# Optimization experiments

Measured on AMD Instinct MI355X. Metric: run time of the kernel, lower is better.

Reference implementation:

```python
import jax, jax.numpy as jnp
import numpy as np

N, C, IN_DIM, H_DIM, NUM_DEP = 16384, 4, 300, 512, 48


def setup_inputs() -> dict:
    key = jax.random.key(0)
    ks = jax.random.split(key, 12)
    # --- tree structure: 4-ary heap, reversed so children have SMALLER index than parent; root = N-1 ---
    i = np.arange(N)
    j = (N - 1) - i                                   # heap index (root j=0)
    cj = C * j[:, None] + 1 + np.arange(C)[None, :]   # heap indices of children [N,C]
    valid = cj <= N - 1
    child_idx = np.where(valid, (N - 1) - cj, 0).astype(np.int32)
    mask_h = valid.astype(np.float32)
    mask_e = valid.astype(np.float32)
    rng = np.random.default_rng(0)
    child_dep = rng.integers(0, NUM_DEP, size=(N, C)).astype(np.int32)
    leaf = ~valid.any(axis=1)
    # torch leaf branch: one virtual child with h=zeros and dep index 0
    mask_e[leaf, 0] = 1.0
    child_dep[leaf, 0] = 0
    child_idx[leaf, 0] = 0
    s = 0.02  # weight scale (stands in for xavier init)
    lin = lambda k, o, d: (jax.random.normal(k, (o, d), jnp.float32) * s)
    return {
        "x": jax.random.normal(ks[0], (N, IN_DIM), jnp.float32),
        "child_idx": jnp.asarray(child_idx),
        "child_dep": jnp.asarray(child_dep),
        "mask_h": jnp.asarray(mask_h),
        "mask_e": jnp.asarray(mask_e),
        "demb": jax.random.normal(ks[1], (NUM_DEP, H_DIM), jnp.float32) * s,
        "iux_w": lin(ks[2], 2 * H_DIM, IN_DIM), "iux_b": jnp.zeros((2 * H_DIM,), jnp.float32),
        "iuh_w": lin(ks[3], 2 * H_DIM, H_DIM), "iuh_b": jnp.zeros((2 * H_DIM,), jnp.float32),
        "iue_w": lin(ks[4], 2 * H_DIM, H_DIM), "iue_b": jnp.zeros((2 * H_DIM,), jnp.float32),
        "fx_w": lin(ks[5], H_DIM, IN_DIM), "fx_b": jnp.zeros((H_DIM,), jnp.float32),
        "fh_w": lin(ks[6], H_DIM, H_DIM), "fh_b": jnp.zeros((H_DIM,), jnp.float32),
        "fe_w": lin(ks[7], H_DIM, H_DIM), "fe_b": jnp.zeros((H_DIM,), jnp.float32),
    }


def reference(x, child_idx, child_dep, mask_h, mask_e, demb,
              iux_w, iux_b, iuh_w, iuh_b, iue_w, iue_b,
              fx_w, fx_b, fh_w, fh_b, fe_w, fe_b):
    n, h_dim = x.shape[0], fh_w.shape[0]

    def step(H, xs):
        t, xt, cidx, cdep, mh, me = xs
        ch = H[cidx] * mh[:, None]            # [C,h] child hiddens (zeros for pad / leaf virtual child)
        e = demb[cdep]                        # [C,h] dependency embeddings
        h_sum = ch.sum(0)                     # child-sum h
        e_sum = (e * me[:, None]).sum(0)      # child-sum dep embedding (leaf -> demb[0])
        iu = (xt @ iux_w.T + iux_b) + (h_sum @ iuh_w.T + iuh_b) + (e_sum @ iue_w.T + iue_b)
        i_g = jax.nn.sigmoid(iu[:h_dim])
        u = jnp.tanh(iu[h_dim:])
        f = jax.nn.sigmoid(ch @ fh_w.T + fh_b + (xt @ fx_w.T + fx_b) + e @ fe_w.T + fe_b)  # [C,h]
        h_new = jnp.tanh(i_g * u + (f * ch).sum(0))   # padded rows contribute 0 since ch=0
        return H.at[t].set(h_new), None

    H0 = jnp.zeros((n, h_dim), x.dtype)
    xs = (jnp.arange(n), x, child_idx, child_dep, mask_h, mask_e)
    Hf, _ = jax.lax.scan(step, H0, xs)
    return Hf[n - 1][None, :]   # root hidden state, shape [1, h_dim]
```

## Files before the change

kernel.cpp:

```cpp
#include <hip/hip_runtime.h>
#include <cstddef>

#define N_NODES 16384
#define HD      512
#define INDIM   300
#define INP     320
#define NDEP    48
#define KT      32
#define LM      16
#define LCOL    128

typedef unsigned int u32;
typedef unsigned short u16;
typedef __attribute__((ext_vector_type(8))) short short8;
typedef __attribute__((ext_vector_type(4))) float f32x4;

typedef __attribute__((address_space(1))) const u32 as1_u32;
typedef __attribute__((address_space(3))) u32 as3_u32;

__device__ __forceinline__ float sigmoidf_(float v) {
    return 1.f / (1.f + __expf(-v));
}
__device__ __forceinline__ float tanhf_(float v) {
    v = fminf(15.f, fmaxf(-15.f, v));
    const float e = __expf(2.f * v);
    return (e - 1.f) / (e + 1.f);
}
__device__ __forceinline__ u16 f2bf(float f) {
    u32 u = __float_as_uint(f);
    u32 r = (u + 0x7fffu + ((u >> 16) & 1u)) >> 16;
    return (u16)r;
}

__global__ __launch_bounds__(256)
void emb_proj_kernel(const float* __restrict__ demb,
                     const float* __restrict__ iue_w,
                     const float* __restrict__ fe_w,
                     const float* __restrict__ iux_b,
                     const float* __restrict__ iuh_b,
                     const float* __restrict__ iue_b,
                     const float* __restrict__ fx_b,
                     const float* __restrict__ fh_b,
                     const float* __restrict__ fe_b,
                     float* __restrict__ iemb,
                     float* __restrict__ femb,
                     float* __restrict__ ibc,
                     float* __restrict__ fbc)
{
    const int bo  = blockIdx.x;
    const int tid = threadIdx.x;
    if (bo == 384) {
        for (int o = tid; o < 1024; o += 256) ibc[o] = iux_b[o] + iuh_b[o] + iue_b[o];
        for (int o = tid; o < 512;  o += 256) fbc[o] = fx_b[o] + fh_b[o] + fe_b[o];
        return;
    }
    const int wave = tid >> 6;
    const int d    = tid & 63;
    const bool isI = (bo < 256);
    const int o    = (isI ? bo : bo - 256) * 4 + wave;
    const float* wrow = isI ? (iue_w + (size_t)o * HD) : (fe_w + (size_t)o * HD);
    if (d >= NDEP) return;
    const float* drow = demb + (size_t)d * HD;

    float4 a0 = make_float4(0.f, 0.f, 0.f, 0.f);
    float4 a1 = make_float4(0.f, 0.f, 0.f, 0.f);
    for (int k = 0; k < HD; k += 8) {
        const float4 wv0 = *reinterpret_cast<const float4*>(wrow + k);
        const float4 wv1 = *reinterpret_cast<const float4*>(wrow + k + 4);
        const float4 dv0 = *reinterpret_cast<const float4*>(drow + k);
        const float4 dv1 = *reinterpret_cast<const float4*>(drow + k + 4);
        a0.x = fmaf(dv0.x, wv0.x, a0.x); a0.y = fmaf(dv0.y, wv0.y, a0.y);
        a0.z = fmaf(dv0.z, wv0.z, a0.z); a0.w = fmaf(dv0.w, wv0.w, a0.w);
        a1.x = fmaf(dv1.x, wv1.x, a1.x); a1.y = fmaf(dv1.y, wv1.y, a1.y);
        a1.z = fmaf(dv1.z, wv1.z, a1.z); a1.w = fmaf(dv1.w, wv1.w, a1.w);
    }
    const float s = ((a0.x + a0.y) + (a0.z + a0.w)) + ((a1.x + a1.y) + (a1.z + a1.w));
    if (isI) iemb[(size_t)d * 1024 + o] = s;
    else     femb[(size_t)d * 512  + o] = s;
}

__global__ __launch_bounds__(256)
void convert_pack_kernel(const float* __restrict__ w1, const float* __restrict__ w2,
                         u16* __restrict__ out, int n1, int K, int Kp, int total)
{
    const int idx = blockIdx.x * 256 + threadIdx.x;
    if (idx >= total) return;
    const int r = idx / Kp, k = idx - r * Kp;
    float v = 0.f;
    if (k < K) v = (r < n1) ? w1[(size_t)r * K + k] : w2[(size_t)(r - n1) * K + k];
    out[idx] = f2bf(v);
}

__device__ __forceinline__
void gemm_body(u16* As, u16* Bs,
               const u16* __restrict__ A, int lda,
               const u16* __restrict__ B, int ldb,
               float* __restrict__ C, int ldc,
               int M, int K, int bx, int by)
{
    const int tid  = threadIdx.x;
    const int lane = tid & 63;
    const int wave = tid >> 6;
    const int mBlk = bx * 128;
    const int nBlk = by * 128;

    const int wr = (wave >> 1) * 64;
    const int wc = (wave & 1) * 64;
    const int fr = lane & 15;
    const int kg = lane >> 4;

    f32x4 acc[4][4];
    #pragma unroll
    for (int i = 0; i < 4; ++i)
        #pragma unroll
        for (int j = 0; j < 4; ++j) acc[i][j] = (f32x4){0.f, 0.f, 0.f, 0.f};

    int offA[4], offB[4];
    #pragma unroll
    for (int it = 0; it < 4; ++it) {
        const int s   = it * 256 + tid;
        const int row = s >> 3, c = s & 7;
        const int cs  = c ^ (row & 7);
        int ga = mBlk + row; if (ga > M - 1) ga = M - 1;
        offA[it] = ga * lda + cs * 8;
        offB[it] = (nBlk + row) * ldb + cs * 8;
    }

    for (int k0 = 0; k0 < K; k0 += 64) {
        #pragma unroll
        for (int it = 0; it < 4; ++it) {
            const int ldsOff = (it * 256 + wave * 64) * 8;
            __builtin_amdgcn_global_load_lds((as1_u32*)(A + offA[it] + k0),
                                             (as3_u32*)(&As[ldsOff]), 16, 0, 0);
            __builtin_amdgcn_global_load_lds((as1_u32*)(B + offB[it] + k0),
                                             (as3_u32*)(&Bs[ldsOff]), 16, 0, 0);
        }
        __syncthreads();
        #pragma unroll
        for (int half = 0; half < 2; ++half) {
            const int ckb = half * 4 + kg;
            short8 af[4], bf[4];
            #pragma unroll
            for (int f = 0; f < 4; ++f) {
                const int ar = wr + f * 16 + fr;
                af[f] = *(const short8*)&As[ar * 64 + ((ckb ^ (ar & 7)) * 8)];
                const int br = wc + f * 16 + fr;
                bf[f] = *(const short8*)&Bs[br * 64 + ((ckb ^ (br & 7)) * 8)];
            }
            #pragma unroll
            for (int mi = 0; mi < 4; ++mi)
                #pragma unroll
                for (int ni = 0; ni < 4; ++ni)
                    acc[mi][ni] = __builtin_amdgcn_mfma_f32_16x16x32_bf16(
                                      af[mi], bf[ni], acc[mi][ni], 0, 0, 0);
        }
        __syncthreads();
    }

    #pragma unroll
    for (int mi = 0; mi < 4; ++mi) {
        const int r0 = mBlk + wr + mi * 16 + kg * 4;
        #pragma unroll
        for (int v = 0; v < 4; ++v) {
            const int r = r0 + v;
            if (r >= M) continue;
            float* crow = C + (size_t)r * ldc + nBlk + wc + fr;
            #pragma unroll
            for (int ni = 0; ni < 4; ++ni)
                crow[ni * 16] = acc[mi][ni][v];
        }
    }
}

__global__ __launch_bounds__(256, 2)
void gemm_bf16_kernel(const u16* __restrict__ A, int lda,
                      const u16* __restrict__ B, int ldb,
                      float* __restrict__ C, int ldc,
                      int M, int K)
{
    __shared__ u16 As[128 * 64];
    __shared__ u16 Bs[128 * 64];
    gemm_body(As, Bs, A, lda, B, ldb, C, ldc, M, K, blockIdx.x, blockIdx.y);
}

__global__ __launch_bounds__(256, 2)
void gemm_bf16_dual_kernel(const u16* __restrict__ A1, int lda1,
                           const u16* __restrict__ B1, int ldb1,
                           float* __restrict__ C1, int ldc1, int M1, int K1,
                           int gx1, int n1,
                           const u16* __restrict__ A2, int lda2,
                           const u16* __restrict__ B2, int ldb2,
                           float* __restrict__ C2, int ldc2, int M2, int K2,
                           int gx2)
{
    __shared__ u16 As[128 * 64];
    __shared__ u16 Bs[128 * 64];
    const int flat = blockIdx.x;
    if (flat < n1) {
        gemm_body(As, Bs, A1, lda1, B1, ldb1, C1, ldc1, M1, K1,
                  flat % gx1, flat / gx1);
    } else {
        const int f2 = flat - n1;
        gemm_body(As, Bs, A2, lda2, B2, ldb2, C2, ldc2, M2, K2,
                  f2 % gx2, f2 / gx2);
    }
}

__global__ __launch_bounds__(256)
void leaf_kernel(const float* __restrict__ XP, const float* __restrict__ iemb,
                 const float* __restrict__ ibc, float* __restrict__ H,
                 u16* __restrict__ Hb)
{
    const int t = blockIdx.x;
    int j = threadIdx.x;
    #pragma unroll
    for (int rep = 0; rep < 2; ++rep, j += 256) {
        const float iu_i = XP[(size_t)t * 1536 + j]       + iemb[j]       + ibc[j];
        const float iu_u = XP[(size_t)t * 1536 + 512 + j] + iemb[512 + j] + ibc[512 + j];
        const float h = tanhf_(sigmoidf_(iu_i) * tanhf_(iu_u));
        H[(size_t)t * 512 + j]  = h;
        Hb[(size_t)t * 512 + j] = f2bf(h);
    }
}

__global__ __launch_bounds__(256)
void hsum_kernel(const float* __restrict__ H, const int* __restrict__ cidx,
                 const float* __restrict__ mh, u16* __restrict__ HSB, int lo)
{
    const int t = lo + blockIdx.x;
    int ci[4]; float m4[4];
    #pragma unroll
    for (int c = 0; c < 4; ++c) { ci[c] = cidx[t * 4 + c]; m4[c] = mh[t * 4 + c]; }
    int j = threadIdx.x;
    #pragma unroll
    for (int rep = 0; rep < 2; ++rep, j += 256) {
        float s = 0.f;
        #pragma unroll
        for (int c = 0; c < 4; ++c)
            if (m4[c] != 0.f) s += m4[c] * H[(size_t)ci[c] * 512 + j];
        HSB[(size_t)blockIdx.x * 512 + j] = f2bf(s);
    }
}

__global__ __launch_bounds__(256)
void combine_kernel(const float* __restrict__ XP, const float* __restrict__ PIU,
                    const float* __restrict__ GF,
                    const int* __restrict__ cidx, const int* __restrict__ cdep,
                    const float* __restrict__ mh, const float* __restrict__ me,
                    const float* __restrict__ iemb, const float* __restrict__ femb,
                    const float* __restrict__ ibc, const float* __restrict__ fbc,
                    float* __restrict__ H, u16* __restrict__ Hb, int lo)
{
    const int t = lo + blockIdx.x;
    int ci[4], dp[4]; float m4[4], e4[4];
    #pragma unroll
    for (int c = 0; c < 4; ++c) {
        ci[c] = cidx[t * 4 + c]; dp[c] = cdep[t * 4 + c];
        m4[c] = mh[t * 4 + c];   e4[c] = me[t * 4 + c];
    }
    int j = threadIdx.x;
    #pragma unroll
    for (int rep = 0; rep < 2; ++rep, j += 256) {
        float ei = 0.f, eu = 0.f;
        #pragma unroll
        for (int c = 0; c < 4; ++c)
            if (e4[c] != 0.f) {
                const float* ie = iemb + (size_t)dp[c] * 1024;
                ei += e4[c] * ie[j];
                eu += e4[c] * ie[512 + j];
            }
        const float iu_i = XP[(size_t)t * 1536 + j] + PIU[(size_t)blockIdx.x * 1024 + j]
                         + ibc[j] + ei;
        const float iu_u = XP[(size_t)t * 1536 + 512 + j] + PIU[(size_t)blockIdx.x * 1024 + 512 + j]
                         + ibc[512 + j] + eu;
        const float xf = XP[(size_t)t * 1536 + 1024 + j] + fbc[j];
        float fcs = 0.f;
        #pragma unroll
        for (int c = 0; c < 4; ++c)
            if (m4[c] != 0.f) {
                const float fv = GF[(size_t)ci[c] * 512 + j] + xf + femb[(size_t)dp[c] * 512 + j];
                fcs += sigmoidf_(fv) * (m4[c] * H[(size_t)ci[c] * 512 + j]);
            }
        const float h = tanhf_(sigmoidf_(iu_i) * tanhf_(iu_u) + fcs);
        H[(size_t)t * 512 + j]  = h;
        Hb[(size_t)t * 512 + j] = f2bf(h);
    }
}

__global__ void copy_out_kernel(const float* __restrict__ H, float* __restrict__ out) {
    const int j = blockIdx.x * 256 + threadIdx.x;
    if (j < HD) out[j] = H[(size_t)(N_NODES - 1) * HD + j];
}

__global__ __launch_bounds__(256)
void emb_setup_kernel(const float* __restrict__ demb,
                      const float* __restrict__ iue_w,
                      const float* __restrict__ fe_w,
                      const float* __restrict__ iux_b,
                      const float* __restrict__ iuh_b,
                      const float* __restrict__ iue_b,
                      const float* __restrict__ fx_b,
                      const float* __restrict__ fh_b,
                      const float* __restrict__ fe_b,
                      float* __restrict__ iemb,
                      float* __restrict__ femb,
                      float* __restrict__ ibc,
                      float* __restrict__ fbc)
{
    const int d   = blockIdx.x;
    const int tid = threadIdx.x;
    __shared__ float sd[HD];
    sd[tid]       = demb[d * HD + tid];
    sd[tid + 256] = demb[d * HD + 256 + tid];
    __syncthreads();

    #pragma unroll
    for (int r = 0; r < 4; ++r) {
        const int o = r * 256 + tid;
        const float* w = iue_w + (size_t)o * HD;
        float acc = 0.f;
        for (int k = 0; k < HD; k += 4) {
            const float4 wv = *reinterpret_cast<const float4*>(w + k);
            acc += sd[k] * wv.x + sd[k + 1] * wv.y + sd[k + 2] * wv.z + sd[k + 3] * wv.w;
        }
        iemb[(size_t)d * 1024 + o] = acc;
    }
    #pragma unroll
    for (int r = 0; r < 2; ++r) {
        const int o = r * 256 + tid;
        const float* w = fe_w + (size_t)o * HD;
        float acc = 0.f;
        for (int k = 0; k < HD; k += 4) {
            const float4 wv = *reinterpret_cast<const float4*>(w + k);
            acc += sd[k] * wv.x + sd[k + 1] * wv.y + sd[k + 2] * wv.z + sd[k + 3] * wv.w;
        }
        femb[(size_t)d * HD + o] = acc;
    }
    if (d == 0) {
        #pragma unroll
        for (int r = 0; r < 4; ++r) { const int o = r * 256 + tid; ibc[o] = iux_b[o] + iuh_b[o] + iue_b[o]; }
        #pragma unroll
        for (int r = 0; r < 2; ++r) { const int o = r * 256 + tid; fbc[o] = fx_b[o] + fh_b[o] + fe_b[o]; }
    }
}

__global__ __launch_bounds__(256, 2)
void level_kernel(const float* __restrict__ x,
                  const int*   __restrict__ child_idx,
                  const int*   __restrict__ child_dep,
                  const float* __restrict__ mask_h,
                  const float* __restrict__ mask_e,
                  const float* __restrict__ iux_w,
                  const float* __restrict__ iuh_w,
                  const float* __restrict__ fx_w,
                  const float* __restrict__ fh_w,
                  const float* __restrict__ iemb,
                  const float* __restrict__ femb,
                  const float* __restrict__ ibc,
                  const float* __restrict__ fbc,
                  float* __restrict__ H,
                  int tLo, int tEnd)
{
    __shared__ __align__(16) float sA[KT][68];
    __shared__ float sWI[KT][LCOL + 1];
    __shared__ float sWU[KT][LCOL + 1];
    __shared__ float sWF[KT][LCOL + 1];
    __shared__ int   sCidx[LM][4];
    __shared__ float sMh[LM][4];
    __shared__ int   sDep[LM][4];
    __shared__ float sMe[LM][4];

    const int tid  = threadIdx.x;
    const int base = tLo + blockIdx.x * LM;
    const int j0   = blockIdx.y * LCOL;

    if (tid < LM * 4) {
        const int m = tid >> 2, c = tid & 3;
        const int t = base + m;
        const bool v = (t < tEnd);
        sCidx[m][c] = v ? child_idx[t * 4 + c] : 0;
        sMh[m][c]   = v ? mask_h[t * 4 + c]    : 0.f;
        sDep[m][c]  = v ? child_dep[t * 4 + c] : 0;
        sMe[m][c]   = v ? mask_e[t * 4 + c]    : 0.f;
    }

    const int jj = tid & 63;
    const int mg = tid >> 6;

    float acc_i[4][2], acc_u[4][2], acc_fx[4][2], acc_f[4][2][4];
    #pragma unroll
    for (int mm = 0; mm < 4; ++mm)
        #pragma unroll
        for (int c2 = 0; c2 < 2; ++c2) {
            acc_i[mm][c2] = 0.f; acc_u[mm][c2] = 0.f; acc_fx[mm][c2] = 0.f;
            #pragma unroll
            for (int c = 0; c < 4; ++c) acc_f[mm][c2][c] = 0.f;
        }

    __syncthreads();

    for (int k0 = 0; k0 < HD; k0 += KT) {
        #pragma unroll
        for (int it = 0; it < 2; ++it) {
            const int chunk = tid + it * 256;
            const int mc = chunk >> 3;
            const int kk = (chunk & 7) * 4;
            const int m = mc >> 2, c = mc & 3;
            const float mh = sMh[m][c];
            float4 v = make_float4(0.f, 0.f, 0.f, 0.f);
            if (mh != 0.f)
                v = *reinterpret_cast<const float4*>(H + (size_t)sCidx[m][c] * HD + k0 + kk);
            sA[kk + 0][mc] = v.x; sA[kk + 1][mc] = v.y; sA[kk + 2][mc] = v.z; sA[kk + 3][mc] = v.w;
        }
        #pragma unroll
        for (int it = 0; it < 4; ++it) {
            const int chunk = tid + it * 256;
            const int row = chunk >> 3;
            const int kk = (chunk & 7) * 4;
            const float4 vI = *reinterpret_cast<const float4*>(iuh_w + (size_t)(j0 + row) * HD + k0 + kk);
            const float4 vU = *reinterpret_cast<const float4*>(iuh_w + (size_t)(j0 + row + 512) * HD + k0 + kk);
            const float4 vF = *reinterpret_cast<const float4*>(fh_w  + (size_t)(j0 + row) * HD + k0 + kk);
            sWI[kk + 0][row] = vI.x; sWI[kk + 1][row] = vI.y; sWI[kk + 2][row] = vI.z; sWI[kk + 3][row] = vI.w;
            sWU[kk + 0][row] = vU.x; sWU[kk + 1][row] = vU.y; sWU[kk + 2][row] = vU.z; sWU[kk + 3][row] = vU.w;
            sWF[kk + 0][row] = vF.x; sWF[kk + 1][row] = vF.y; sWF[kk + 2][row] = vF.z; sWF[kk + 3][row] = vF.w;
        }
        __syncthreads();
        #pragma unroll 4
        for (int k = 0; k < KT; ++k) {
            const float wi0 = sWI[k][jj], wi1 = sWI[k][jj + 64];
            const float wu0 = sWU[k][jj], wu1 = sWU[k][jj + 64];
            const float wf0 = sWF[k][jj], wf1 = sWF[k][jj + 64];
            #pragma unroll
            for (int mm = 0; mm < 4; ++mm) {
                const int m = mg + mm * 4;
                const float4 cv = *reinterpret_cast<const float4*>(&sA[k][m * 4]);
                const float hs = (cv.x + cv.y) + (cv.z + cv.w);
                acc_i[mm][0] = fmaf(hs, wi0, acc_i[mm][0]);
                acc_i[mm][1] = fmaf(hs, wi1, acc_i[mm][1]);
                acc_u[mm][0] = fmaf(hs, wu0, acc_u[mm][0]);
                acc_u[mm][1] = fmaf(hs, wu1, acc_u[mm][1]);
                acc_f[mm][0][0] = fmaf(cv.x, wf0, acc_f[mm][0][0]);
                acc_f[mm][1][0] = fmaf(cv.x, wf1, acc_f[mm][1][0]);
                acc_f[mm][0][1] = fmaf(cv.y, wf0, acc_f[mm][0][1]);
                acc_f[mm][1][1] = fmaf(cv.y, wf1, acc_f[mm][1][1]);
                acc_f[mm][0][2] = fmaf(cv.z, wf0, acc_f[mm][0][2]);
                acc_f[mm][1][2] = fmaf(cv.z, wf1, acc_f[mm][1][2]);
                acc_f[mm][0][3] = fmaf(cv.w, wf0, acc_f[mm][0][3]);
                acc_f[mm][1][3] = fmaf(cv.w, wf1, acc_f[mm][1][3]);
            }
        }
        __syncthreads();
    }

    for (int k0 = 0; k0 < INDIM; k0 += KT) {
        if (tid < 128) {
            const int m = tid >> 3;
            const int kk = (tid & 7) * 4;
            const int t = base + m;
            float4 v = make_float4(0.f, 0.f, 0.f, 0.f);
            if (t < tEnd && (k0 + kk + 3) < INDIM)
                v = *reinterpret_cast<const float4*>(x + (size_t)t * INDIM + k0 + kk);
            sA[kk + 0][m] = v.x; sA[kk + 1][m] = v.y; sA[kk + 2][m] = v.z; sA[kk + 3][m] = v.w;
        }
        #pragma unroll
        for (int it = 0; it < 4; ++it) {
            const int chunk = tid + it * 256;
            const int row = chunk >> 3;
            const int kk = (chunk & 7) * 4;
            float4 vI = make_float4(0.f, 0.f, 0.f, 0.f), vU = vI, vF = vI;
            if ((k0 + kk + 3) < INDIM) {
                vI = *reinterpret_cast<const float4*>(iux_w + (size_t)(j0 + row) * INDIM + k0 + kk);
                vU = *reinterpret_cast<const float4*>(iux_w + (size_t)(j0 + row + 512) * INDIM + k0 + kk);
                vF = *reinterpret_cast<const float4*>(fx_w  + (size_t)(j0 + row) * INDIM + k0 + kk);
            }
            sWI[kk + 0][row] = vI.x; sWI[kk + 1][row] = vI.y; sWI[kk + 2][row] = vI.z; sWI[kk + 3][row] = vI.w;
            sWU[kk + 0][row] = vU.x; sWU[kk + 1][row] = vU.y; sWU[kk + 2][row] = vU.z; sWU[kk + 3][row] = vU.w;
            sWF[kk + 0][row] = vF.x; sWF[kk + 1][row] = vF.y; sWF[kk + 2][row] = vF.z; sWF[kk + 3][row] = vF.w;
        }
        __syncthreads();
        #pragma unroll 4
        for (int k = 0; k < KT; ++k) {
            const float wi0 = sWI[k][jj], wi1 = sWI[k][jj + 64];
            const float wu0 = sWU[k][jj], wu1 = sWU[k][jj + 64];
            const float wf0 = sWF[k][jj], wf1 = sWF[k][jj + 64];
            #pragma unroll
            for (int mm = 0; mm < 4; ++mm) {
                const float xv = sA[k][mg + mm * 4];
                acc_i[mm][0]  = fmaf(xv, wi0, acc_i[mm][0]);
                acc_i[mm][1]  = fmaf(xv, wi1, acc_i[mm][1]);
                acc_u[mm][0]  = fmaf(xv, wu0, acc_u[mm][0]);
                acc_u[mm][1]  = fmaf(xv, wu1, acc_u[mm][1]);
                acc_fx[mm][0] = fmaf(xv, wf0, acc_fx[mm][0]);
                acc_fx[mm][1] = fmaf(xv, wf1, acc_fx[mm][1]);
            }
        }
        __syncthreads();
    }

    #pragma unroll
    for (int mm = 0; mm < 4; ++mm) {
        const int m = mg + mm * 4;
        const int t = base + m;
        if (t >= tEnd) continue;
        #pragma unroll
        for (int c2 = 0; c2 < 2; ++c2) {
            const int j = j0 + c2 * 64 + jj;
            float emb_i = 0.f, emb_u = 0.f;
            #pragma unroll
            for (int c = 0; c < 4; ++c) {
                const float mev = sMe[m][c];
                if (mev != 0.f) {
                    const float* ie = iemb + (size_t)sDep[m][c] * 1024;
                    emb_i = fmaf(mev, ie[j], emb_i);
                    emb_u = fmaf(mev, ie[j + 512], emb_u);
                }
            }
            const float iu_i = acc_i[mm][c2] + ibc[j] + emb_i;
            const float iu_u = acc_u[mm][c2] + ibc[j + 512] + emb_u;
            const float ig = sigmoidf_(iu_i);
            const float uu = tanhf_(iu_u);
            float fcs = 0.f;
            #pragma unroll
            for (int c = 0; c < 4; ++c) {
                const float mh = sMh[m][c];
                if (mh != 0.f) {
                    const float fv = acc_f[mm][c2][c] + acc_fx[mm][c2] + fbc[j]
                                   + femb[(size_t)sDep[m][c] * HD + j];
                    const float fg = sigmoidf_(fv);
                    const float chj = H[(size_t)sCidx[m][c] * HD + j] * mh;
                    fcs = fmaf(fg, chj, fcs);
                }
            }
            H[(size_t)t * HD + j] = tanhf_(fmaf(ig, uu, fcs));
        }
    }
}

static const int lvlLo[8] = {0, 10923, 15019, 16043, 16299, 16363, 16379, 16383};
static const int lvlN[8]  = {10923, 4096, 1024, 256, 64, 16, 4, 1};

extern "C" void kernel_launch(void* const* d_in, const int* in_sizes, int n_in,
                              void* d_out, int out_size, void* d_ws, size_t ws_size,
                              hipStream_t stream)
{
    const float* x     = (const float*)d_in[0];
    const int*   cidx  = (const int*)  d_in[1];
    const int*   cdep  = (const int*)  d_in[2];
    const float* mh    = (const float*)d_in[3];
    const float* me    = (const float*)d_in[4];
    const float* demb  = (const float*)d_in[5];
    const float* iux_w = (const float*)d_in[6];
    const float* iux_b = (const float*)d_in[7];
    const float* iuh_w = (const float*)d_in[8];
    const float* iuh_b = (const float*)d_in[9];
    const float* iue_w = (const float*)d_in[10];
    const float* iue_b = (const float*)d_in[11];
    const float* fx_w  = (const float*)d_in[12];
    const float* fx_b  = (const float*)d_in[13];
    const float* fh_w  = (const float*)d_in[14];
    const float* fh_b  = (const float*)d_in[15];
    const float* fe_w  = (const float*)d_in[16];
    const float* fe_b  = (const float*)d_in[17];

    const size_t szH   = 33554432;
    const size_t szHb  = 16777216;
    const size_t szXP  = 100663296;
    const size_t szGF  = 33554432;
    const size_t szPIU = 16777216;
    const size_t szHSB = 4194304;
    const size_t szXB  = 10485760;
    const size_t szWX  = 983040;
    const size_t szWH  = 1572864;
    const size_t szIE  = 196608, szFE = 98304, szIB = 4096, szFB = 2048;
    const size_t need = szH + szHb + szXP + szGF + szPIU + szHSB + szXB + szWX + szWH
                      + szIE + szFE + szIB + szFB;

    if (ws_size >= need) {
        char* w = (char*)d_ws;
        float* H    = (float*)w;  w += szH;
        u16*   Hb   = (u16*)w;    w += szHb;
        float* XP   = (float*)w;  w += szXP;
        float* GF   = (float*)w;  w += szGF;
        float* PIU  = (float*)w;  w += szPIU;
        u16*   HSB  = (u16*)w;    w += szHSB;
        u16*   xb   = (u16*)w;    w += szXB;
        u16*   WXb  = (u16*)w;    w += szWX;
        u16*   WHb  = (u16*)w;    w += szWH;
        float* iemb = (float*)w;  w += szIE;
        float* femb = (float*)w;  w += szFE;
        float* ibc  = (float*)w;  w += szIB;
        float* fbc  = (float*)w;  w += szFB;

        {
            const int tot = N_NODES * INP;
            hipLaunchKernelGGL(convert_pack_kernel, dim3((tot + 255) / 256), dim3(256), 0, stream,
                               x, x, xb, N_NODES, INDIM, INP, tot);
        }
        {
            const int tot = 1536 * INP;
            hipLaunchKernelGGL(convert_pack_kernel, dim3((tot + 255) / 256), dim3(256), 0, stream,
                               iux_w, fx_w, WXb, 1024, INDIM, INP, tot);
        }
        {
            const int tot = 1536 * HD;
            hipLaunchKernelGGL(convert_pack_kernel, dim3((tot + 255) / 256), dim3(256), 0, stream,
                               iuh_w, fh_w, WHb, 1024, HD, HD, tot);
        }
        hipLaunchKernelGGL(emb_proj_kernel, dim3(385), dim3(256), 0, stream,
                           demb, iue_w, fe_w, iux_b, iuh_b, iue_b, fx_b, fh_b, fe_b,
                           iemb, femb, ibc, fbc);

        hipLaunchKernelGGL(gemm_bf16_kernel, dim3(N_NODES / 128, 1536 / 128), dim3(256), 0, stream,
                           xb, INP, WXb, INP, XP, 1536, N_NODES, INP);

        hipLaunchKernelGGL(leaf_kernel, dim3(lvlN[0]), dim3(256), 0, stream, XP, iemb, ibc, H, Hb);

        for (int l = 1; l < 8; ++l) {
            const int pLo = lvlLo[l - 1], pN = lvlN[l - 1];
            const int lo  = lvlLo[l],     n  = lvlN[l];
            hipLaunchKernelGGL(hsum_kernel, dim3(n), dim3(256), 0, stream, H, cidx, mh, HSB, lo);
            const int gx1 = (pN + 127) / 128, n1 = gx1 * (512 / 128);
            const int gx2 = (n + 127) / 128,  n2 = gx2 * (1024 / 128);
            hipLaunchKernelGGL(gemm_bf16_dual_kernel, dim3(n1 + n2), dim3(256), 0, stream,
                               Hb + (size_t)pLo * HD, HD, WHb + (size_t)1024 * HD, HD,
                               GF + (size_t)pLo * HD, HD, pN, HD, gx1, n1,
                               HSB, HD, WHb, HD, PIU, 1024, n, HD, gx2);
            hipLaunchKernelGGL(combine_kernel, dim3(n), dim3(256), 0, stream,
                               XP, PIU, GF, cidx, cdep, mh, me, iemb, femb, ibc, fbc, H, Hb, lo);
        }
        hipLaunchKernelGGL(copy_out_kernel, dim3(2), dim3(256), 0, stream, H, (float*)d_out);
        return;
    }

    float* ws   = (float*)d_ws;
    float* H    = ws;
    float* iemb = H + (size_t)N_NODES * HD;
    float* femb = iemb + (size_t)NDEP * 1024;
    float* ibc  = femb + (size_t)NDEP * HD;
    float* fbc  = ibc + 1024;

    hipLaunchKernelGGL(emb_setup_kernel, dim3(NDEP), dim3(256), 0, stream,
                       demb, iue_w, fe_w, iux_b, iuh_b, iue_b, fx_b, fh_b, fe_b,
                       iemb, femb, ibc, fbc);
    for (int l = 0; l < 8; ++l) {
        dim3 grid((lvlN[l] + LM - 1) / LM, HD / LCOL);
        hipLaunchKernelGGL(level_kernel, grid, dim3(256), 0, stream,
                           x, cidx, cdep, mh, me, iux_w, iuh_w, fx_w, fh_w,
                           iemb, femb, ibc, fbc, H, lvlLo[l], lvlLo[l] + lvlN[l]);
    }
    hipLaunchKernelGGL(copy_out_kernel, dim3(2), dim3(256), 0, stream, H, (float*)d_out);
}
```

Baseline: 267.5 us.

## Fuse child-sum into combine, store GEMM outputs as bf16, merge conversion launches

Each level's combine is now launched per parent of the next level, computing its children's hidden states and writing the child-sum straight into the next GEMM's input. This removes the separate hsum kernel, the leaf kernel, the copy-out kernel and two of three conversion launches. GEMM outputs (XP, GF, PIU) are stored as bf16, and the forget-gate x projection is computed only for non-leaf rows, which cuts memory traffic. The cost is extra rounding in the intermediates, plus less parallelism in the upper levels, since one block now handles up to four children one after another.

```diff
diff --git a/kernel.cpp b/kernel.cpp
--- a/kernel.cpp
+++ b/kernel.cpp
@@ -6,6 +6,7 @@
 #define INDIM   300
 #define INP     320
 #define NDEP    48
+#define NLEAF   10923
 #define KT      32
 #define LM      16
 #define LCOL    128
@@ -30,6 +31,12 @@
     u32 u = __float_as_uint(f);
     u32 r = (u + 0x7fffu + ((u >> 16) & 1u)) >> 16;
     return (u16)r;
+}
+__device__ __forceinline__ float b2f(u16 v) {
+    return __uint_as_float((u32)v << 16);
+}
+__device__ __forceinline__ u32 pack2(float a, float b) {
+    return (u32)f2bf(a) | ((u32)f2bf(b) << 16);
 }
 
 __global__ __launch_bounds__(256)
@@ -79,23 +86,41 @@
     else     femb[(size_t)d * 512  + o] = s;
 }
 
+#define CV_T0 (N_NODES * INP)
+#define CV_T1 (1536 * INP)
+#define CV_T2 (1536 * HD)
+
 __global__ __launch_bounds__(256)
-void convert_pack_kernel(const float* __restrict__ w1, const float* __restrict__ w2,
-                         u16* __restrict__ out, int n1, int K, int Kp, int total)
+void convert_all_kernel(const float* __restrict__ x,
+                        const float* __restrict__ iux_w, const float* __restrict__ fx_w,
+                        const float* __restrict__ iuh_w, const float* __restrict__ fh_w,
+                        u16* __restrict__ xb, u16* __restrict__ WXb, u16* __restrict__ WHb)
 {
     const int idx = blockIdx.x * 256 + threadIdx.x;
-    if (idx >= total) return;
-    const int r = idx / Kp, k = idx - r * Kp;
-    float v = 0.f;
-    if (k < K) v = (r < n1) ? w1[(size_t)r * K + k] : w2[(size_t)(r - n1) * K + k];
-    out[idx] = f2bf(v);
+    if (idx < CV_T0) {
+        const int r = idx / INP, k = idx - r * INP;
+        xb[idx] = f2bf(k < INDIM ? x[(size_t)r * INDIM + k] : 0.f);
+    } else if (idx < CV_T0 + CV_T1) {
+        const int i2 = idx - CV_T0;
+        const int r = i2 / INP, k = i2 - r * INP;
+        float v = 0.f;
+        if (k < INDIM) v = (r < 1024) ? iux_w[(size_t)r * INDIM + k]
+                                      : fx_w[(size_t)(r - 1024) * INDIM + k];
+        WXb[i2] = f2bf(v);
+    } else {
+        const int i3 = idx - CV_T0 - CV_T1;
+        const int r = i3 >> 9, k = i3 & 511;
+        const float v = (r < 1024) ? iuh_w[(size_t)r * HD + k]
+                                   : fh_w[(size_t)(r - 1024) * HD + k];
+        WHb[i3] = f2bf(v);
+    }
 }
 
 __device__ __forceinline__
 void gemm_body(u16* As, u16* Bs,
                const u16* __restrict__ A, int lda,
                const u16* __restrict__ B, int ldb,
-               float* __restrict__ C, int ldc,
+               u16* __restrict__ C, int ldc,
                int M, int K, int bx, int by)
 {
     const int tid  = threadIdx.x;
@@ -164,33 +189,22 @@
         for (int v = 0; v < 4; ++v) {
             const int r = r0 + v;
             if (r >= M) continue;
-            float* crow = C + (size_t)r * ldc + nBlk + wc + fr;
+            u16* crow = C + (size_t)r * ldc + nBlk + wc + fr;
             #pragma unroll
             for (int ni = 0; ni < 4; ++ni)
-                crow[ni * 16] = acc[mi][ni][v];
-        }
-    }
-}
-
-__global__ __launch_bounds__(256, 2)
-void gemm_bf16_kernel(const u16* __restrict__ A, int lda,
-                      const u16* __restrict__ B, int ldb,
-                      float* __restrict__ C, int ldc,
-                      int M, int K)
-{
-    __shared__ u16 As[128 * 64];
-    __shared__ u16 Bs[128 * 64];
-    gemm_body(As, Bs, A, lda, B, ldb, C, ldc, M, K, blockIdx.x, blockIdx.y);
+                crow[ni * 16] = f2bf(acc[mi][ni][v]);
+        }
+    }
 }
 
 __global__ __launch_bounds__(256, 2)
 void gemm_bf16_dual_kernel(const u16* __restrict__ A1, int lda1,
                            const u16* __restrict__ B1, int ldb1,
-                           float* __restrict__ C1, int ldc1, int M1, int K1,
+                           u16* __restrict__ C1, int ldc1, int M1, int K1,
                            int gx1, int n1,
                            const u16* __restrict__ A2, int lda2,
                            const u16* __restrict__ B2, int ldb2,
-                           float* __restrict__ C2, int ldc2, int M2, int K2,
+                           u16* __restrict__ C2, int ldc2, int M2, int K2,
                            int gx2)
 {
     __shared__ u16 As[128 * 64];
@@ -207,89 +221,131 @@
 }
 
 __global__ __launch_bounds__(256)
-void leaf_kernel(const float* __restrict__ XP, const float* __restrict__ iemb,
-                 const float* __restrict__ ibc, float* __restrict__ H,
-                 u16* __restrict__ Hb)
-{
-    const int t = blockIdx.x;
-    int j = threadIdx.x;
-    #pragma unroll
-    for (int rep = 0; rep < 2; ++rep, j += 256) {
-        const float iu_i = XP[(size_t)t * 1536 + j]       + iemb[j]       + ibc[j];
-        const float iu_u = XP[(size_t)t * 1536 + 512 + j] + iemb[512 + j] + ibc[512 + j];
-        const float h = tanhf_(sigmoidf_(iu_i) * tanhf_(iu_u));
-        H[(size_t)t * 512 + j]  = h;
-        Hb[(size_t)t * 512 + j] = f2bf(h);
-    }
+void fused_leaf_kernel(const u16* __restrict__ XPiub,
+                       const float* __restrict__ iemb, const float* __restrict__ ibc,
+                       const int* __restrict__ cidx, const float* __restrict__ mh,
+                       float* __restrict__ H, u16* __restrict__ Hb,
+                       u16* __restrict__ HSB, int loNext)
+{
+    const int g   = blockIdx.x;
+    const int p   = loNext + g;
+    const int j2  = threadIdx.x * 2;
+
+    int ct[4]; float cm[4];
+    #pragma unroll
+    for (int c = 0; c < 4; ++c) { ct[c] = cidx[p * 4 + c]; cm[c] = mh[p * 4 + c]; }
+
+    const float2 ibci = *reinterpret_cast<const float2*>(&ibc[j2]);
+    const float2 ibcu = *reinterpret_cast<const float2*>(&ibc[512 + j2]);
+    const float2 iei  = *reinterpret_cast<const float2*>(&iemb[j2]);
+    const float2 ieu  = *reinterpret_cast<const float2*>(&iemb[512 + j2]);
+
+    float hs0 = 0.f, hs1 = 0.f;
+    #pragma unroll
+    for (int c = 0; c < 4; ++c) {
+        if (cm[c] == 0.f) continue;
+        const int t = ct[c];
+        const u32 xi = *reinterpret_cast<const u32*>(&XPiub[(size_t)t * 1024 + j2]);
+        const u32 xu = *reinterpret_cast<const u32*>(&XPiub[(size_t)t * 1024 + 512 + j2]);
+        const float h0 = tanhf_(sigmoidf_(b2f((u16)xi) + iei.x + ibci.x)
+                                * tanhf_(b2f((u16)xu) + ieu.x + ibcu.x));
+        const float h1 = tanhf_(sigmoidf_(b2f((u16)(xi >> 16)) + iei.y + ibci.y)
+                                * tanhf_(b2f((u16)(xu >> 16)) + ieu.y + ibcu.y));
+        *reinterpret_cast<float2*>(&H[(size_t)t * 512 + j2]) = make_float2(h0, h1);
+        *reinterpret_cast<u32*>(&Hb[(size_t)t * 512 + j2]) = pack2(h0, h1);
+        hs0 += h0; hs1 += h1;
+    }
+    *reinterpret_cast<u32*>(&HSB[(size_t)g * 512 + j2]) = pack2(hs0, hs1);
 }
 
 __global__ __launch_bounds__(256)
-void hsum_kernel(const float* __restrict__ H, const int* __restrict__ cidx,
-                 const float* __restrict__ mh, u16* __restrict__ HSB, int lo)
-{
-    const int t = lo + blockIdx.x;
-    int ci[4]; float m4[4];
-    #pragma unroll
-    for (int c = 0; c < 4; ++c) { ci[c] = cidx[t * 4 + c]; m4[c] = mh[t * 4 + c]; }
-    int j = threadIdx.x;
-    #pragma unroll
-    for (int rep = 0; rep < 2; ++rep, j += 256) {
-        float s = 0.f;
-        #pragma unroll
-        for (int c = 0; c < 4; ++c)
-            if (m4[c] != 0.f) s += m4[c] * H[(size_t)ci[c] * 512 + j];
-        HSB[(size_t)blockIdx.x * 512 + j] = f2bf(s);
-    }
-}
-
-__global__ __launch_bounds__(256)
-void combine_kernel(const float* __restrict__ XP, const float* __restrict__ PIU,
-                    const float* __restrict__ GF,
-                    const int* __restrict__ cidx, const int* __restrict__ cdep,
-                    const float* __restrict__ mh, const float* __restrict__ me,
-                    const float* __restrict__ iemb, const float* __restrict__ femb,
-                    const float* __restrict__ ibc, const float* __restrict__ fbc,
-                    float* __restrict__ H, u16* __restrict__ Hb, int lo)
-{
-    const int t = lo + blockIdx.x;
-    int ci[4], dp[4]; float m4[4], e4[4];
+void fused_combine_kernel(const u16* __restrict__ XPiub, const u16* __restrict__ XPfb,
+                          const u16* __restrict__ PIUb, const u16* __restrict__ GFb,
+                          const int* __restrict__ cidx, const int* __restrict__ cdep,
+                          const float* __restrict__ mh, const float* __restrict__ me,
+                          const float* __restrict__ iemb, const float* __restrict__ femb,
+                          const float* __restrict__ ibc, const float* __restrict__ fbc,
+                          float* __restrict__ H, u16* __restrict__ Hb,
+                          u16* __restrict__ HSB,
+                          int lo, int loNext, int isRoot, float* __restrict__ outp)
+{
+    const int j2 = threadIdx.x * 2;
+
+    int ct[4]; float cm[4];
+    if (isRoot) {
+        ct[0] = N_NODES - 1; cm[0] = 1.f;
+        ct[1] = ct[2] = ct[3] = 0; cm[1] = cm[2] = cm[3] = 0.f;
+    } else {
+        const int p = loNext + blockIdx.x;
+        #pragma unroll
+        for (int c = 0; c < 4; ++c) { ct[c] = cidx[p * 4 + c]; cm[c] = mh[p * 4 + c]; }
+    }
+
+    const float2 ibci = *reinterpret_cast<const float2*>(&ibc[j2]);
+    const float2 ibcu = *reinterpret_cast<const float2*>(&ibc[512 + j2]);
+    const float2 fbc2 = *reinterpret_cast<const float2*>(&fbc[j2]);
+
+    float hs0 = 0.f, hs1 = 0.f;
     #pragma unroll
     for (int c = 0; c < 4; ++c) {
-        ci[c] = cidx[t * 4 + c]; dp[c] = cdep[t * 4 + c];
-        m4[c] = mh[t * 4 + c];   e4[c] = me[t * 4 + c];
-    }
-    int j = threadIdx.x;
-    #pragma unroll
-    for (int rep = 0; rep < 2; ++rep, j += 256) {
-        float ei = 0.f, eu = 0.f;
-        #pragma unroll
-        for (int c = 0; c < 4; ++c)
-            if (e4[c] != 0.f) {
-                const float* ie = iemb + (size_t)dp[c] * 1024;
-                ei += e4[c] * ie[j];
-                eu += e4[c] * ie[512 + j];
+        if (cm[c] == 0.f) continue;
+        const int t = ct[c];
+
+        int ci2[4], dp2[4]; float m2[4], e2[4];
+        #pragma unroll
+        for (int k = 0; k < 4; ++k) {
+            ci2[k] = cidx[t * 4 + k]; dp2[k] = cdep[t * 4 + k];
+            m2[k]  = mh[t * 4 + k];   e2[k]  = me[t * 4 + k];
+        }
+
+        float ei0 = 0.f, ei1 = 0.f, eu0 = 0.f, eu1 = 0.f;
+        #pragma unroll
+        for (int k = 0; k < 4; ++k) {
+            if (e2[k] != 0.f) {
+                const float* ie = iemb + (size_t)dp2[k] * 1024;
+                const float2 a = *reinterpret_cast<const float2*>(&ie[j2]);
+                const float2 b = *reinterpret_cast<const float2*>(&ie[512 + j2]);
+                ei0 = fmaf(e2[k], a.x, ei0); ei1 = fmaf(e2[k], a.y, ei1);
+                eu0 = fmaf(e2[k], b.x, eu0); eu1 = fmaf(e2[k], b.y, eu1);
             }
-        const float iu_i = XP[(size_t)t * 1536 + j] + PIU[(size_t)blockIdx.x * 1024 + j]
-                         + ibc[j] + ei;
-        const float iu_u = XP[(size_t)t * 1536 + 512 + j] + PIU[(size_t)blockIdx.x * 1024 + 512 + j]
-                         + ibc[512 + j] + eu;
-        const float xf = XP[(size_t)t * 1536 + 1024 + j] + fbc[j];
-        float fcs = 0.f;
-        #pragma unroll
-        for (int c = 0; c < 4; ++c)
-            if (m4[c] != 0.f) {
-                const float fv = GF[(size_t)ci[c] * 512 + j] + xf + femb[(size_t)dp[c] * 512 + j];
-                fcs += sigmoidf_(fv) * (m4[c] * H[(size_t)ci[c] * 512 + j]);
+        }
+
+        const u32 xi = *reinterpret_cast<const u32*>(&XPiub[(size_t)t * 1024 + j2]);
+        const u32 xu = *reinterpret_cast<const u32*>(&XPiub[(size_t)t * 1024 + 512 + j2]);
+        const u32 pi = *reinterpret_cast<const u32*>(&PIUb[(size_t)(t - lo) * 1024 + j2]);
+        const u32 pu = *reinterpret_cast<const u32*>(&PIUb[(size_t)(t - lo) * 1024 + 512 + j2]);
+        const u32 xf = *reinterpret_cast<const u32*>(&XPfb[(size_t)(t - NLEAF) * 512 + j2]);
+
+        const float iu_i0 = b2f((u16)xi) + b2f((u16)pi) + ibci.x + ei0;
+        const float iu_i1 = b2f((u16)(xi >> 16)) + b2f((u16)(pi >> 16)) + ibci.y + ei1;
+        const float iu_u0 = b2f((u16)xu) + b2f((u16)pu) + ibcu.x + eu0;
+        const float iu_u1 = b2f((u16)(xu >> 16)) + b2f((u16)(pu >> 16)) + ibcu.y + eu1;
+        const float xf0 = b2f((u16)xf) + fbc2.x;
+        const float xf1 = b2f((u16)(xf >> 16)) + fbc2.y;
+
+        float fcs0 = 0.f, fcs1 = 0.f;
+        #pragma unroll
+        for (int k = 0; k < 4; ++k) {
+            if (m2[k] != 0.f) {
+                const u32 gf = *reinterpret_cast<const u32*>(&GFb[(size_t)ci2[k] * 512 + j2]);
+                const float2 fe = *reinterpret_cast<const float2*>(&femb[(size_t)dp2[k] * 512 + j2]);
+                const float2 hc = *reinterpret_cast<const float2*>(&H[(size_t)ci2[k] * 512 + j2]);
+                const float fv0 = b2f((u16)gf) + xf0 + fe.x;
+                const float fv1 = b2f((u16)(gf >> 16)) + xf1 + fe.y;
+                fcs0 = fmaf(sigmoidf_(fv0), m2[k] * hc.x, fcs0);
+                fcs1 = fmaf(sigmoidf_(fv1), m2[k] * hc.y, fcs1);
             }
-        const float h = tanhf_(sigmoidf_(iu_i) * tanhf_(iu_u) + fcs);
-        H[(size_t)t * 512 + j]  = h;
-        Hb[(size_t)t * 512 + j] = f2bf(h);
-    }
-}
-
-__global__ void copy_out_kernel(const float* __restrict__ H, float* __restrict__ out) {
-    const int j = blockIdx.x * 256 + threadIdx.x;
-    if (j < HD) out[j] = H[(size_t)(N_NODES - 1) * HD + j];
+        }
+
+        const float h0 = tanhf_(fmaf(sigmoidf_(iu_i0), tanhf_(iu_u0), fcs0));
+        const float h1 = tanhf_(fmaf(sigmoidf_(iu_i1), tanhf_(iu_u1), fcs1));
+        *reinterpret_cast<float2*>(&H[(size_t)t * 512 + j2]) = make_float2(h0, h1);
+        *reinterpret_cast<u32*>(&Hb[(size_t)t * 512 + j2]) = pack2(h0, h1);
+        hs0 += h0; hs1 += h1;
+        if (isRoot) *reinterpret_cast<float2*>(&outp[j2]) = make_float2(h0, h1);
+    }
+    if (!isRoot)
+        *reinterpret_cast<u32*>(&HSB[(size_t)blockIdx.x * 512 + j2]) = pack2(hs0, hs1);
 }
 
 __global__ __launch_bounds__(256)
@@ -406,9 +462,9 @@
             const int mc = chunk >> 3;
             const int kk = (chunk & 7) * 4;
             const int m = mc >> 2, c = mc & 3;
-            const float mh = sMh[m][c];
+            const float mhv = sMh[m][c];
             float4 v = make_float4(0.f, 0.f, 0.f, 0.f);
-            if (mh != 0.f)
+            if (mhv != 0.f)
                 v = *reinterpret_cast<const float4*>(H + (size_t)sCidx[m][c] * HD + k0 + kk);
             sA[kk + 0][mc] = v.x; sA[kk + 1][mc] = v.y; sA[kk + 2][mc] = v.z; sA[kk + 3][mc] = v.w;
         }
@@ -522,18 +578,23 @@
             float fcs = 0.f;
             #pragma unroll
             for (int c = 0; c < 4; ++c) {
-                const float mh = sMh[m][c];
-                if (mh != 0.f) {
+                const float mhv = sMh[m][c];
+                if (mhv != 0.f) {
                     const float fv = acc_f[mm][c2][c] + acc_fx[mm][c2] + fbc[j]
                                    + femb[(size_t)sDep[m][c] * HD + j];
                     const float fg = sigmoidf_(fv);
-                    const float chj = H[(size_t)sCidx[m][c] * HD + j] * mh;
+                    const float chj = H[(size_t)sCidx[m][c] * HD + j] * mhv;
                     fcs = fmaf(fg, chj, fcs);
                 }
             }
             H[(size_t)t * HD + j] = tanhf_(fmaf(ig, uu, fcs));
         }
     }
+}
+
+__global__ void copy_out_kernel(const float* __restrict__ H, float* __restrict__ out) {
+    const int j = blockIdx.x * 256 + threadIdx.x;
+    if (j < HD) out[j] = H[(size_t)(N_NODES - 1) * HD + j];
 }
 
 static const int lvlLo[8] = {0, 10923, 15019, 16043, 16299, 16363, 16379, 16383};
@@ -562,73 +623,78 @@
     const float* fe_w  = (const float*)d_in[16];
     const float* fe_b  = (const float*)d_in[17];
 
-    const size_t szH   = 33554432;
-    const size_t szHb  = 16777216;
-    const size_t szXP  = 100663296;
-    const size_t szGF  = 33554432;
-    const size_t szPIU = 16777216;
-    const size_t szHSB = 4194304;
-    const size_t szXB  = 10485760;
-    const size_t szWX  = 983040;
-    const size_t szWH  = 1572864;
-    const size_t szIE  = 196608, szFE = 98304, szIB = 4096, szFB = 2048;
-    const size_t need = szH + szHb + szXP + szGF + szPIU + szHSB + szXB + szWX + szWH
-                      + szIE + szFE + szIB + szFB;
+    const size_t szH   = (size_t)N_NODES * HD * 4;
+    const size_t szHb  = (size_t)N_NODES * HD * 2;
+    const size_t szXPi = (size_t)N_NODES * 1024 * 2;
+    const size_t szXPf = (size_t)5461 * 512 * 2;
+    const size_t szGF  = (size_t)N_NODES * HD * 2;
+    const size_t szPIU = (size_t)4096 * 1024 * 2;
+    const size_t szHSB = (size_t)4096 * 512 * 2;
+    const size_t szXB  = (size_t)N_NODES * INP * 2;
+    const size_t szWX  = (size_t)1536 * INP * 2;
+    const size_t szWH  = (size_t)1536 * HD * 2;
+    const size_t szIE  = (size_t)NDEP * 1024 * 4;
+    const size_t szFE  = (size_t)NDEP * 512 * 4;
+    const size_t szIB  = 4096, szFB = 2048;
+    const size_t need = szH + szHb + szXPi + szXPf + szGF + szPIU + szHSB
+                      + szXB + szWX + szWH + szIE + szFE + szIB + szFB;
 
     if (ws_size >= need) {
         char* w = (char*)d_ws;
-        float* H    = (float*)w;  w += szH;
-        u16*   Hb   = (u16*)w;    w += szHb;
-        float* XP   = (float*)w;  w += szXP;
-        float* GF   = (float*)w;  w += szGF;
-        float* PIU  = (float*)w;  w += szPIU;
-        u16*   HSB  = (u16*)w;    w += szHSB;
-        u16*   xb   = (u16*)w;    w += szXB;
-        u16*   WXb  = (u16*)w;    w += szWX;
-        u16*   WHb  = (u16*)w;    w += szWH;
-        float* iemb = (float*)w;  w += szIE;
-        float* femb = (float*)w;  w += szFE;
-        float* ibc  = (float*)w;  w += szIB;
-        float* fbc  = (float*)w;  w += szFB;
+        float* H     = (float*)w;  w += szH;
+        u16*   Hb    = (u16*)w;    w += szHb;
+        u16*   XPiub = (u16*)w;    w += szXPi;
+        u16*   XPfb  = (u16*)w;    w += szXPf;
+        u16*   GFb   = (u16*)w;    w += szGF;
+        u16*   PIUb  = (u16*)w;    w += szPIU;
+        u16*   HSB   = (u16*)w;    w += szHSB;
+        u16*   xb    = (u16*)w;    w += szXB;
+        u16*   WXb   = (u16*)w;    w += szWX;
+        u16*   WHb   = (u16*)w;    w += szWH;
+        float* iemb  = (float*)w;  w += szIE;
+        float* femb  = (float*)w;  w += szFE;
+        float* ibc   = (float*)w;  w += szIB;
+        float* fbc   = (float*)w;  w += szFB;
 
         {
-            const int tot = N_NODES * INP;
-            hipLaunchKernelGGL(convert_pack_kernel, dim3((tot + 255) / 256), dim3(256), 0, stream,
-                               x, x, xb, N_NODES, INDIM, INP, tot);
-        }
-        {
-            const int tot = 1536 * INP;
-            hipLaunchKernelGGL(convert_pack_kernel, dim3((tot + 255) / 256), dim3(256), 0, stream,
-                               iux_w, fx_w, WXb, 1024, INDIM, INP, tot);
-        }
-        {
-            const int tot = 1536 * HD;
-            hipLaunchKernelGGL(convert_pack_kernel, dim3((tot + 255) / 256), dim3(256), 0, stream,
-                               iuh_w, fh_w, WHb, 1024, HD, HD, tot);
+            const int tot = CV_T0 + CV_T1 + CV_T2;
+            hipLaunchKernelGGL(convert_all_kernel, dim3((tot + 255) / 256), dim3(256), 0, stream,
+                               x, iux_w, fx_w, iuh_w, fh_w, xb, WXb, WHb);
         }
         hipLaunchKernelGGL(emb_proj_kernel, dim3(385), dim3(256), 0, stream,
                            demb, iue_w, fe_w, iux_b, iuh_b, iue_b, fx_b, fh_b, fe_b,
                            iemb, femb, ibc, fbc);
 
-        hipLaunchKernelGGL(gemm_bf16_kernel, dim3(N_NODES / 128, 1536 / 128), dim3(256), 0, stream,
-                           xb, INP, WXb, INP, XP, 1536, N_NODES, INP);
-
-        hipLaunchKernelGGL(leaf_kernel, dim3(lvlN[0]), dim3(256), 0, stream, XP, iemb, ibc, H, Hb);
+        {
+            const int gx1 = N_NODES / 128, n1 = gx1 * (1024 / 128);
+            const int gx2 = (5461 + 127) / 128;
+            const int n2  = gx2 * (512 / 128);
+            hipLaunchKernelGGL(gemm_bf16_dual_kernel, dim3(n1 + n2), dim3(256), 0, stream,
+                               xb, INP, WXb, INP, XPiub, 1024, N_NODES, INP, gx1, n1,
+                               xb + (size_t)NLEAF * INP, INP, WXb + (size_t)1024 * INP, INP,
+                               XPfb, 512, 5461, INP, gx2);
+        }
+
+        hipLaunchKernelGGL(fused_leaf_kernel, dim3(lvlN[1]), dim3(256), 0, stream,
+                           XPiub, iemb, ibc, cidx, mh, H, Hb, HSB, lvlLo[1]);
 
         for (int l = 1; l < 8; ++l) {
             const int pLo = lvlLo[l - 1], pN = lvlN[l - 1];
             const int lo  = lvlLo[l],     n  = lvlN[l];
-            hipLaunchKernelGGL(hsum_kernel, dim3(n), dim3(256), 0, stream, H, cidx, mh, HSB, lo);
             const int gx1 = (pN + 127) / 128, n1 = gx1 * (512 / 128);
             const int gx2 = (n + 127) / 128,  n2 = gx2 * (1024 / 128);
             hipLaunchKernelGGL(gemm_bf16_dual_kernel, dim3(n1 + n2), dim3(256), 0, stream,
                                Hb + (size_t)pLo * HD, HD, WHb + (size_t)1024 * HD, HD,
-                               GF + (size_t)pLo * HD, HD, pN, HD, gx1, n1,
-                               HSB, HD, WHb, HD, PIU, 1024, n, HD, gx2);
-            hipLaunchKernelGGL(combine_kernel, dim3(n), dim3(256), 0, stream,
-                               XP, PIU, GF, cidx, cdep, mh, me, iemb, femb, ibc, fbc, H, Hb, lo);
-        }
-        hipLaunchKernelGGL(copy_out_kernel, dim3(2), dim3(256), 0, stream, H, (float*)d_out);
+                               GFb + (size_t)pLo * HD, HD, pN, HD, gx1, n1,
+                               HSB, HD, WHb, HD, PIUb, 1024, n, HD, gx2);
+            const int isRoot = (l == 7);
+            const int gridC  = isRoot ? 1 : lvlN[l + 1];
+            const int loNext = isRoot ? 0 : lvlLo[l + 1];
+            hipLaunchKernelGGL(fused_combine_kernel, dim3(gridC), dim3(256), 0, stream,
+                               XPiub, XPfb, PIUb, GFb, cidx, cdep, mh, me,
+                               iemb, femb, ibc, fbc, H, Hb, HSB,
+                               lo, loNext, isRoot, (float*)d_out);
+        }
         return;
     }
 
```

After: 248.6 us. -7.1%, faster.
